# Kernel tuning notes

Hardware: AMD Instinct MI355X
Metric: run time of the kernel (lower is better)

## Reference

```python
import jax, jax.numpy as jnp
import numpy as np

B, N, K, H, NHEADS = 2, 2000, 32, 128, 4
EPS = 1e-6


def setup_inputs() -> dict:
    key = jax.random.key(0)
    ks = jax.random.split(key, 16)
    h_V = jax.random.normal(ks[0], (B, N, H), jnp.float32)
    h_EV = jax.random.normal(ks[1], (B, N, K, 2 * H), jnp.float32)
    h_KV = jax.random.normal(ks[2], (B, N, K, H), jnp.float32)
    h_KE = jax.random.normal(ks[3], (B, N, K, H), jnp.float32)
    mask_V = jax.random.randint(ks[4], (B, N), 0, 2).astype(jnp.float32)
    mask_attend = jax.random.randint(ks[5], (B, N, K), 0, 2).astype(jnp.float32)
    # guarantee at least one valid neighbor per node so masked softmax is finite
    mask_attend = mask_attend.at[:, :, 0].set(1.0)
    s = 1.0 / np.sqrt(H)
    W_Q = jax.random.normal(ks[6], (H, H), jnp.float32) * s
    W_K1 = jax.random.normal(ks[7], (H, H), jnp.float32) * s
    W_K2 = jax.random.normal(ks[8], (H, H), jnp.float32) * s
    W_V = jax.random.normal(ks[9], (H, 2 * H), jnp.float32) * s
    W_O = jax.random.normal(ks[10], (H, H), jnp.float32) * s
    gain = jnp.ones((H,), jnp.float32)
    bias = jnp.zeros((H,), jnp.float32)
    return dict(h_V=h_V, h_EV=h_EV, h_KV=h_KV, h_KE=h_KE, mask_V=mask_V,
                mask_attend=mask_attend, W_Q=W_Q, W_K1=W_K1, W_K2=W_K2,
                W_V=W_V, W_O=W_O, gain=gain, bias=bias)


def reference(h_V, h_EV, h_KV, h_KE, mask_V, mask_attend,
              W_Q, W_K1, W_K2, W_V, W_O, gain, bias):
    d = H // NHEADS  # per-head dim
    # Linear layers (torch Linear: x @ W.T), split heads
    Q = (h_V @ W_Q.T).reshape(B, N, 1, NHEADS, d)        # [B,N,1,h,d]
    K1 = (h_KE @ W_K1.T).reshape(B, N, K, NHEADS, d)     # [B,N,K,h,d]
    K2 = (h_KV @ W_K2.T).reshape(B, N, K, NHEADS, d)
    V = (h_EV @ W_V.T).reshape(B, N, K, NHEADS, d)
    # QKK: elementwise triple product reduced over d -> [B,N,K,h] -> [B,N,h,K]
    logits = jnp.sum(Q * K1 * K2, axis=-1)
    logits = jnp.swapaxes(logits, -2, -1) / d            # [B,N,h,K]
    # masked softmax over neighbors
    mask = jnp.broadcast_to(mask_attend[:, :, None, :], logits.shape)
    neg_inf = jnp.float32(np.finfo(np.float32).min)
    attend = jax.nn.softmax(jnp.where(mask > 0, logits, neg_inf), axis=-1)
    attend = mask * attend
    # aggregate neighbors per head, merge heads, output projection
    h_up = jnp.einsum('bnhk,bnkhd->bnhd', attend, V).reshape(B, N, H)
    dh = h_up @ W_O.T
    # residual + Normalize (torch .var is unbiased -> ddof=1)
    x = h_V + dh
    mu = x.mean(-1, keepdims=True)
    sigma = jnp.sqrt(x.var(-1, ddof=1, keepdims=True) + EPS)
    out = gain * (x - mu) / (sigma + EPS) + bias
    return mask_V[..., None] * out
```

## Files before the change

kernel.cpp:

```cpp
#include <hip/hip_runtime.h>
#include <hip/hip_bf16.h>
#include <math.h>

#define BN_TOTAL 4000
#define NODES 4
#define KN 32
#define HD 128
#define NH 4

typedef unsigned short ushort_t;
typedef unsigned int u32;
typedef short bf16x8 __attribute__((ext_vector_type(8)));
typedef float f32x4  __attribute__((ext_vector_type(4)));

__device__ __forceinline__ float bf2f(ushort_t u) {
    return __uint_as_float(((u32)u) << 16);
}
__device__ __forceinline__ ushort_t f2bf(float f) {
    u32 u = __float_as_uint(f);
    u += 0x7FFFu + ((u >> 16) & 1u);
    return (ushort_t)(u >> 16);
}
__device__ __forceinline__ u32 pack2bf(float lo, float hi) {
    return ((u32)f2bf(hi) << 16) | (u32)f2bf(lo);
}
__device__ __forceinline__ void cvt8(uint4 w, float* f) {
    f[0] = __uint_as_float(w.x << 16); f[1] = __uint_as_float(w.x & 0xFFFF0000u);
    f[2] = __uint_as_float(w.y << 16); f[3] = __uint_as_float(w.y & 0xFFFF0000u);
    f[4] = __uint_as_float(w.z << 16); f[5] = __uint_as_float(w.z & 0xFFFF0000u);
    f[6] = __uint_as_float(w.w << 16); f[7] = __uint_as_float(w.w & 0xFFFF0000u);
}

template<bool ISBF>
__device__ __forceinline__ void load8(const void* base, int idx, float* f) {
    if (ISBF) {
        uint4 v = *reinterpret_cast<const uint4*>((const ushort_t*)base + idx);
        cvt8(v, f);
    } else {
        const float* p = (const float*)base + idx;
        float4 a = *reinterpret_cast<const float4*>(p);
        float4 b = *reinterpret_cast<const float4*>(p + 4);
        f[0] = a.x; f[1] = a.y; f[2] = a.z; f[3] = a.w;
        f[4] = b.x; f[5] = b.y; f[6] = b.z; f[7] = b.w;
    }
}
template<bool ISBF>
__device__ __forceinline__ float load1(const void* base, int idx) {
    return ISBF ? bf2f(((const ushort_t*)base)[idx]) : ((const float*)base)[idx];
}
template<bool ISBF>
__device__ __forceinline__ bf16x8 loadfrag(const void* base, int idx) {
    if (ISBF) {
        return *reinterpret_cast<const bf16x8*>((const ushort_t*)base + idx);
    } else {
        const float* p = (const float*)base + idx;
        float4 a = *reinterpret_cast<const float4*>(p);
        float4 b = *reinterpret_cast<const float4*>(p + 4);
        bf16x8 r;
        r[0] = (short)f2bf(a.x); r[1] = (short)f2bf(a.y);
        r[2] = (short)f2bf(a.z); r[3] = (short)f2bf(a.w);
        r[4] = (short)f2bf(b.x); r[5] = (short)f2bf(b.y);
        r[6] = (short)f2bf(b.z); r[7] = (short)f2bf(b.w);
        return r;
    }
}

template<bool ISBF>
__device__ __forceinline__ void stage_chunk(const void* W, int elem_off, u32* sW,
                                            int chunk, int lane) {
    if (ISBF) {
        uint4 v = *reinterpret_cast<const uint4*>((const ushort_t*)W + elem_off);
        *reinterpret_cast<uint4*>(sW + chunk * 256 + lane * 4) = v;
    } else {
        const float* p = (const float*)W + elem_off;
        float4 a = *reinterpret_cast<const float4*>(p);
        float4 b = *reinterpret_cast<const float4*>(p + 4);
        uint4 v;
        v.x = pack2bf(a.x, a.y); v.y = pack2bf(a.z, a.w);
        v.z = pack2bf(b.x, b.y); v.w = pack2bf(b.z, b.w);
        *reinterpret_cast<uint4*>(sW + chunk * 256 + lane * 4) = v;
    }
}
__device__ __forceinline__ bf16x8 read_frag(const u32* sW, int chunk, int lane) {
    return *reinterpret_cast<const bf16x8*>(
        reinterpret_cast<const ushort_t*>(sW) + chunk * 512 + lane * 8);
}

template<bool ISBF>
__device__ __forceinline__ void run4(
    const void* h_V, const void* h_EV, const void* h_KV, const void* h_KE,
    const void* mask_V, const void* mask_att,
    const void* W_Q, const void* W_K1, const void* W_K2,
    const void* W_Vw, const void* W_O, const void* gain, const void* bias,
    void* out,
    u32* sW, float* shV, float* sQ, float* sLog, float* sAtt, float* sHU)
{
    const int t    = threadIdx.x;
    const int w    = t >> 6;
    const int lane = t & 63;
    const int quad = lane >> 4;
    const int lr   = lane & 15;
    const int node = blockIdx.x * NODES + w;
    const int c1   = lane, c2 = lane + 64;

    const float mA1 = load1<ISBF>(mask_att, node * KN + lr);
    const float mA2 = load1<ISBF>(mask_att, node * KN + 16 + lr);
    const float mV  = load1<ISBF>(mask_V, node);
    const float gn1 = load1<ISBF>(gain, c1), gn2 = load1<ISBF>(gain, c2);
    const float bs1 = load1<ISBF>(bias, c1), bs2 = load1<ISBF>(bias, c2);

    #pragma unroll
    for (int j = 0; j < 16; ++j) {
        const int c  = w * 16 + j;
        const int ks = (c >> 3) & 3, nt = c & 7;
        const void* W = (c < 32) ? W_K1 : W_K2;
        stage_chunk<ISBF>(W, (nt * 16 + lr) * HD + ks * 32 + quad * 8, sW, c, lane);
    }

    shV[w * HD + 2 * lane]     = load1<ISBF>(h_V, node * HD + 2 * lane);
    shV[w * HD + 2 * lane + 1] = load1<ISBF>(h_V, node * HD + 2 * lane + 1);

    bf16x8 aKE[2][4], aKV[2][4];
    const int aoff = node * KN * HD;
    #pragma unroll
    for (int mt = 0; mt < 2; ++mt)
        #pragma unroll
        for (int ks = 0; ks < 4; ++ks) {
            const int eo = aoff + (mt * 16 + lr) * HD + ks * 32 + quad * 8;
            aKE[mt][ks] = loadfrag<ISBF>(h_KE, eo);
            aKV[mt][ks] = loadfrag<ISBF>(h_KV, eo);
        }
    __syncthreads();

    {
        float q1 = 0.f, q2 = 0.f;
        #pragma unroll 4
        for (int jc = 0; jc < HD; jc += 8) {
            float hv[8];
            #pragma unroll
            for (int j = 0; j < 8; ++j) hv[j] = shV[w * HD + jc + j];
            float w1[8], w2[8];
            load8<ISBF>(W_Q, c1 * HD + jc, w1);
            load8<ISBF>(W_Q, c2 * HD + jc, w2);
            #pragma unroll
            for (int j = 0; j < 8; ++j) { q1 += w1[j] * hv[j]; q2 += w2[j] * hv[j]; }
        }
        sQ[w * HD + c1] = q1;
        sQ[w * HD + c2] = q2;
    }
    __syncthreads();

    float qv[8];
    #pragma unroll
    for (int nt = 0; nt < 8; ++nt) qv[nt] = sQ[w * HD + nt * 16 + lr];

    const f32x4 zero4 = {0.f, 0.f, 0.f, 0.f};
    #pragma unroll
    for (int h = 0; h < NH; ++h) {
        f32x4 a1[2][2], a2[2][2];
        #pragma unroll
        for (int mt = 0; mt < 2; ++mt)
            #pragma unroll
            for (int j = 0; j < 2; ++j) { a1[mt][j] = zero4; a2[mt][j] = zero4; }
        #pragma unroll
        for (int ks = 0; ks < 4; ++ks) {
            #pragma unroll
            for (int j = 0; j < 2; ++j) {
                const int nt = 2 * h + j;
                bf16x8 b1 = read_frag(sW, ks * 8 + nt, lane);
                bf16x8 b2 = read_frag(sW, 32 + ks * 8 + nt, lane);
                #pragma unroll
                for (int mt = 0; mt < 2; ++mt) {
                    a1[mt][j] = __builtin_amdgcn_mfma_f32_16x16x32_bf16(aKE[mt][ks], b1, a1[mt][j], 0, 0, 0);
                    a2[mt][j] = __builtin_amdgcn_mfma_f32_16x16x32_bf16(aKV[mt][ks], b2, a2[mt][j], 0, 0, 0);
                }
            }
        }
        #pragma unroll
        for (int mt = 0; mt < 2; ++mt) {
            #pragma unroll
            for (int r = 0; r < 4; ++r) {
                float p = qv[2 * h] * a1[mt][0][r] * a2[mt][0][r]
                        + qv[2 * h + 1] * a1[mt][1][r] * a2[mt][1][r];
                p += __shfl_xor(p, 1); p += __shfl_xor(p, 2);
                p += __shfl_xor(p, 4); p += __shfl_xor(p, 8);
                if (lr == 0)
                    sLog[w * HD + h * KN + mt * 16 + quad * 4 + r] = p * (1.f / 32.f);
            }
        }
    }
    __syncthreads();

    #pragma unroll
    for (int j = 0; j < 16; ++j) {
        const int c  = w * 16 + j;
        const int ks = c >> 3, nt = c & 7;
        stage_chunk<ISBF>(W_Vw, (nt * 16 + lr) * 256 + ks * 32 + quad * 8, sW, c, lane);
    }
    bf16x8 aEV[2][8];
    const int eoff = node * KN * 256;
    #pragma unroll
    for (int mt = 0; mt < 2; ++mt)
        #pragma unroll
        for (int ks = 0; ks < 8; ++ks)
            aEV[mt][ks] = loadfrag<ISBF>(h_EV, eoff + (mt * 16 + lr) * 256 + ks * 32 + quad * 8);

    {
        const int h = quad;
        float l1 = sLog[w * HD + h * KN + lr];
        float l2 = sLog[w * HD + h * KN + 16 + lr];
        const float NEG = -3.402823466e38f;
        l1 = (mA1 > 0.f) ? l1 : NEG;
        l2 = (mA2 > 0.f) ? l2 : NEG;
        float mx = fmaxf(l1, l2);
        #pragma unroll
        for (int d = 1; d < 16; d <<= 1) mx = fmaxf(mx, __shfl_xor(mx, d));
        float e1 = __expf(l1 - mx), e2 = __expf(l2 - mx);
        float ss = e1 + e2;
        #pragma unroll
        for (int d = 1; d < 16; d <<= 1) ss += __shfl_xor(ss, d);
        float inv = 1.f / ss;
        sAtt[w * HD + h * KN + lr]      = mA1 * e1 * inv;
        sAtt[w * HD + h * KN + 16 + lr] = mA2 * e2 * inv;
    }
    __syncthreads();

    #pragma unroll
    for (int h = 0; h < NH; ++h) {
        f32x4 cv[2][2];
        #pragma unroll
        for (int mt = 0; mt < 2; ++mt)
            #pragma unroll
            for (int j = 0; j < 2; ++j) cv[mt][j] = zero4;
        #pragma unroll
        for (int ks = 0; ks < 8; ++ks) {
            #pragma unroll
            for (int j = 0; j < 2; ++j) {
                bf16x8 b = read_frag(sW, ks * 8 + 2 * h + j, lane);
                #pragma unroll
                for (int mt = 0; mt < 2; ++mt)
                    cv[mt][j] = __builtin_amdgcn_mfma_f32_16x16x32_bf16(aEV[mt][ks], b, cv[mt][j], 0, 0, 0);
            }
        }
        float hu0 = 0.f, hu1 = 0.f;
        #pragma unroll
        for (int mt = 0; mt < 2; ++mt) {
            #pragma unroll
            for (int r = 0; r < 4; ++r) {
                float a = sAtt[w * HD + h * KN + mt * 16 + quad * 4 + r];
                hu0 += a * cv[mt][0][r];
                hu1 += a * cv[mt][1][r];
            }
        }
        hu0 += __shfl_xor(hu0, 16); hu0 += __shfl_xor(hu0, 32);
        hu1 += __shfl_xor(hu1, 16); hu1 += __shfl_xor(hu1, 32);
        if (quad == 0) {
            sHU[w * HD + (2 * h) * 16 + lr]     = hu0;
            sHU[w * HD + (2 * h + 1) * 16 + lr] = hu1;
        }
    }
    __syncthreads();

    {
        float d1 = 0.f, d2 = 0.f;
        #pragma unroll 4
        for (int jc = 0; jc < HD; jc += 8) {
            float hv[8];
            #pragma unroll
            for (int j = 0; j < 8; ++j) hv[j] = sHU[w * HD + jc + j];
            float w1[8], w2[8];
            load8<ISBF>(W_O, c1 * HD + jc, w1);
            load8<ISBF>(W_O, c2 * HD + jc, w2);
            #pragma unroll
            for (int j = 0; j < 8; ++j) { d1 += w1[j] * hv[j]; d2 += w2[j] * hv[j]; }
        }
        float x1 = shV[w * HD + c1] + d1;
        float x2 = shV[w * HD + c2] + d2;
        float s  = x1 + x2;
        float s2 = x1 * x1 + x2 * x2;
        #pragma unroll
        for (int d = 1; d < 64; d <<= 1) {
            s  += __shfl_xor(s, d);
            s2 += __shfl_xor(s2, d);
        }
        float mu    = s * (1.f / 128.f);
        float var   = (s2 - 128.f * mu * mu) * (1.f / 127.f);
        float sigma = sqrtf(var + 1e-6f);
        float inv   = 1.f / (sigma + 1e-6f);
        float o1 = mV * (gn1 * (x1 - mu) * inv + bs1);
        float o2 = mV * (gn2 * (x2 - mu) * inv + bs2);
        if (ISBF) {
            ((ushort_t*)out)[node * HD + c1] = f2bf(o1);
            ((ushort_t*)out)[node * HD + c2] = f2bf(o2);
        } else {
            ((float*)out)[node * HD + c1] = o1;
            ((float*)out)[node * HD + c2] = o2;
        }
    }
}

__global__ __launch_bounds__(256, 2) void spatppi_kernel(
    const void* h_V, const void* h_EV, const void* h_KV, const void* h_KE,
    const void* mask_V, const void* mask_att,
    const void* W_Q, const void* W_K1, const void* W_K2,
    const void* W_Vw, const void* W_O, const void* gain, const void* bias,
    void* out)
{
    __shared__ u32 sW[16384];
    __shared__ float shV[NODES * HD];
    __shared__ float sQ[NODES * HD];
    __shared__ float sLog[NODES * HD];
    __shared__ float sAtt[NODES * HD];
    __shared__ float sHU[NODES * HD];

    const bool isbf = (((const u32*)gain)[0] != 0x3F800000u);
    if (isbf)
        run4<true >(h_V, h_EV, h_KV, h_KE, mask_V, mask_att, W_Q, W_K1, W_K2,
                    W_Vw, W_O, gain, bias, out, sW, shV, sQ, sLog, sAtt, sHU);
    else
        run4<false>(h_V, h_EV, h_KV, h_KE, mask_V, mask_att, W_Q, W_K1, W_K2,
                    W_Vw, W_O, gain, bias, out, sW, shV, sQ, sLog, sAtt, sHU);
}

extern "C" void kernel_launch(void* const* d_in, const int* in_sizes, int n_in,
                              void* d_out, int out_size, void* d_ws, size_t ws_size,
                              hipStream_t stream) {
    spatppi_kernel<<<dim3(BN_TOTAL / NODES), dim3(256), 0, stream>>>(
        d_in[0], d_in[1], d_in[2], d_in[3], d_in[4], d_in[5],
        d_in[6], d_in[7], d_in[8], d_in[9], d_in[10], d_in[11], d_in[12],
        d_out);
}
```

Baseline: 353.7 us.

## Drop LDS weight staging; load MFMA weight fragments from global memory

Removes the 64KB shared-memory weight buffer and all block-wide barriers. Each warp now reads W_K1/W_K2/W_V fragments straight from global (L2-cached) memory and handles one 16-row tile of neighbors at a time to cut register pressure. Launch bounds rise to 4 blocks per SM to raise occupancy. The cost is far more global weight traffic per block, plus an fp32-to-bf16 conversion of the weights on every load in the fp32 path.

```diff
diff --git a/kernel.cpp b/kernel.cpp
--- a/kernel.cpp
+++ b/kernel.cpp
@@ -1,5 +1,4 @@
 #include <hip/hip_runtime.h>
-#include <hip/hip_bf16.h>
 #include <math.h>
 
 #define BN_TOTAL 4000
@@ -20,9 +19,6 @@
     u32 u = __float_as_uint(f);
     u += 0x7FFFu + ((u >> 16) & 1u);
     return (ushort_t)(u >> 16);
-}
-__device__ __forceinline__ u32 pack2bf(float lo, float hi) {
-    return ((u32)f2bf(hi) << 16) | (u32)f2bf(lo);
 }
 __device__ __forceinline__ void cvt8(uint4 w, float* f) {
     f[0] = __uint_as_float(w.x << 16); f[1] = __uint_as_float(w.x & 0xFFFF0000u);
@@ -66,34 +62,13 @@
 }
 
 template<bool ISBF>
-__device__ __forceinline__ void stage_chunk(const void* W, int elem_off, u32* sW,
-                                            int chunk, int lane) {
-    if (ISBF) {
-        uint4 v = *reinterpret_cast<const uint4*>((const ushort_t*)W + elem_off);
-        *reinterpret_cast<uint4*>(sW + chunk * 256 + lane * 4) = v;
-    } else {
-        const float* p = (const float*)W + elem_off;
-        float4 a = *reinterpret_cast<const float4*>(p);
-        float4 b = *reinterpret_cast<const float4*>(p + 4);
-        uint4 v;
-        v.x = pack2bf(a.x, a.y); v.y = pack2bf(a.z, a.w);
-        v.z = pack2bf(b.x, b.y); v.w = pack2bf(b.z, b.w);
-        *reinterpret_cast<uint4*>(sW + chunk * 256 + lane * 4) = v;
-    }
-}
-__device__ __forceinline__ bf16x8 read_frag(const u32* sW, int chunk, int lane) {
-    return *reinterpret_cast<const bf16x8*>(
-        reinterpret_cast<const ushort_t*>(sW) + chunk * 512 + lane * 8);
-}
-
-template<bool ISBF>
 __device__ __forceinline__ void run4(
     const void* h_V, const void* h_EV, const void* h_KV, const void* h_KE,
     const void* mask_V, const void* mask_att,
     const void* W_Q, const void* W_K1, const void* W_K2,
     const void* W_Vw, const void* W_O, const void* gain, const void* bias,
     void* out,
-    u32* sW, float* shV, float* sQ, float* sLog, float* sAtt, float* sHU)
+    float* shV, float* sQ, float* sLog, float* sAtt, float* sHU)
 {
     const int t    = threadIdx.x;
     const int w    = t >> 6;
@@ -105,32 +80,9 @@
 
     const float mA1 = load1<ISBF>(mask_att, node * KN + lr);
     const float mA2 = load1<ISBF>(mask_att, node * KN + 16 + lr);
-    const float mV  = load1<ISBF>(mask_V, node);
-    const float gn1 = load1<ISBF>(gain, c1), gn2 = load1<ISBF>(gain, c2);
-    const float bs1 = load1<ISBF>(bias, c1), bs2 = load1<ISBF>(bias, c2);
-
-    #pragma unroll
-    for (int j = 0; j < 16; ++j) {
-        const int c  = w * 16 + j;
-        const int ks = (c >> 3) & 3, nt = c & 7;
-        const void* W = (c < 32) ? W_K1 : W_K2;
-        stage_chunk<ISBF>(W, (nt * 16 + lr) * HD + ks * 32 + quad * 8, sW, c, lane);
-    }
 
     shV[w * HD + 2 * lane]     = load1<ISBF>(h_V, node * HD + 2 * lane);
     shV[w * HD + 2 * lane + 1] = load1<ISBF>(h_V, node * HD + 2 * lane + 1);
-
-    bf16x8 aKE[2][4], aKV[2][4];
-    const int aoff = node * KN * HD;
-    #pragma unroll
-    for (int mt = 0; mt < 2; ++mt)
-        #pragma unroll
-        for (int ks = 0; ks < 4; ++ks) {
-            const int eo = aoff + (mt * 16 + lr) * HD + ks * 32 + quad * 8;
-            aKE[mt][ks] = loadfrag<ISBF>(h_KE, eo);
-            aKV[mt][ks] = loadfrag<ISBF>(h_KV, eo);
-        }
-    __syncthreads();
 
     {
         float q1 = 0.f, q2 = 0.f;
@@ -148,40 +100,41 @@
         sQ[w * HD + c1] = q1;
         sQ[w * HD + c2] = q2;
     }
-    __syncthreads();
-
     float qv[8];
     #pragma unroll
     for (int nt = 0; nt < 8; ++nt) qv[nt] = sQ[w * HD + nt * 16 + lr];
 
     const f32x4 zero4 = {0.f, 0.f, 0.f, 0.f};
-    #pragma unroll
-    for (int h = 0; h < NH; ++h) {
-        f32x4 a1[2][2], a2[2][2];
-        #pragma unroll
-        for (int mt = 0; mt < 2; ++mt)
-            #pragma unroll
-            for (int j = 0; j < 2; ++j) { a1[mt][j] = zero4; a2[mt][j] = zero4; }
+
+    const int aoff = node * KN * HD;
+    #pragma unroll
+    for (int mt = 0; mt < 2; ++mt) {
+        bf16x8 aKE[4], aKV[4];
         #pragma unroll
         for (int ks = 0; ks < 4; ++ks) {
-            #pragma unroll
-            for (int j = 0; j < 2; ++j) {
-                const int nt = 2 * h + j;
-                bf16x8 b1 = read_frag(sW, ks * 8 + nt, lane);
-                bf16x8 b2 = read_frag(sW, 32 + ks * 8 + nt, lane);
+            const int eo = aoff + (mt * 16 + lr) * HD + ks * 32 + quad * 8;
+            aKE[ks] = loadfrag<ISBF>(h_KE, eo);
+            aKV[ks] = loadfrag<ISBF>(h_KV, eo);
+        }
+        #pragma unroll
+        for (int h = 0; h < NH; ++h) {
+            f32x4 a1[2], a2[2];
+            a1[0] = zero4; a1[1] = zero4; a2[0] = zero4; a2[1] = zero4;
+            #pragma unroll
+            for (int ks = 0; ks < 4; ++ks) {
                 #pragma unroll
-                for (int mt = 0; mt < 2; ++mt) {
-                    a1[mt][j] = __builtin_amdgcn_mfma_f32_16x16x32_bf16(aKE[mt][ks], b1, a1[mt][j], 0, 0, 0);
-                    a2[mt][j] = __builtin_amdgcn_mfma_f32_16x16x32_bf16(aKV[mt][ks], b2, a2[mt][j], 0, 0, 0);
+                for (int j = 0; j < 2; ++j) {
+                    const int wo = ((2 * h + j) * 16 + lr) * HD + ks * 32 + quad * 8;
+                    bf16x8 b1 = loadfrag<ISBF>(W_K1, wo);
+                    bf16x8 b2 = loadfrag<ISBF>(W_K2, wo);
+                    a1[j] = __builtin_amdgcn_mfma_f32_16x16x32_bf16(aKE[ks], b1, a1[j], 0, 0, 0);
+                    a2[j] = __builtin_amdgcn_mfma_f32_16x16x32_bf16(aKV[ks], b2, a2[j], 0, 0, 0);
                 }
             }
-        }
-        #pragma unroll
-        for (int mt = 0; mt < 2; ++mt) {
             #pragma unroll
             for (int r = 0; r < 4; ++r) {
-                float p = qv[2 * h] * a1[mt][0][r] * a2[mt][0][r]
-                        + qv[2 * h + 1] * a1[mt][1][r] * a2[mt][1][r];
+                float p = qv[2 * h] * a1[0][r] * a2[0][r]
+                        + qv[2 * h + 1] * a1[1][r] * a2[1][r];
                 p += __shfl_xor(p, 1); p += __shfl_xor(p, 2);
                 p += __shfl_xor(p, 4); p += __shfl_xor(p, 8);
                 if (lr == 0)
@@ -189,21 +142,6 @@
             }
         }
     }
-    __syncthreads();
-
-    #pragma unroll
-    for (int j = 0; j < 16; ++j) {
-        const int c  = w * 16 + j;
-        const int ks = c >> 3, nt = c & 7;
-        stage_chunk<ISBF>(W_Vw, (nt * 16 + lr) * 256 + ks * 32 + quad * 8, sW, c, lane);
-    }
-    bf16x8 aEV[2][8];
-    const int eoff = node * KN * 256;
-    #pragma unroll
-    for (int mt = 0; mt < 2; ++mt)
-        #pragma unroll
-        for (int ks = 0; ks < 8; ++ks)
-            aEV[mt][ks] = loadfrag<ISBF>(h_EV, eoff + (mt * 16 + lr) * 256 + ks * 32 + quad * 8);
 
     {
         const int h = quad;
@@ -223,35 +161,41 @@
         sAtt[w * HD + h * KN + lr]      = mA1 * e1 * inv;
         sAtt[w * HD + h * KN + 16 + lr] = mA2 * e2 * inv;
     }
-    __syncthreads();
-
-    #pragma unroll
-    for (int h = 0; h < NH; ++h) {
-        f32x4 cv[2][2];
-        #pragma unroll
-        for (int mt = 0; mt < 2; ++mt)
-            #pragma unroll
-            for (int j = 0; j < 2; ++j) cv[mt][j] = zero4;
-        #pragma unroll
-        for (int ks = 0; ks < 8; ++ks) {
-            #pragma unroll
-            for (int j = 0; j < 2; ++j) {
-                bf16x8 b = read_frag(sW, ks * 8 + 2 * h + j, lane);
+
+    const int eoff = node * KN * 256;
+    float hu[NH][2];
+    #pragma unroll
+    for (int h = 0; h < NH; ++h) { hu[h][0] = 0.f; hu[h][1] = 0.f; }
+    #pragma unroll
+    for (int mt = 0; mt < 2; ++mt) {
+        bf16x8 aEV[8];
+        #pragma unroll
+        for (int ks = 0; ks < 8; ++ks)
+            aEV[ks] = loadfrag<ISBF>(h_EV, eoff + (mt * 16 + lr) * 256 + ks * 32 + quad * 8);
+        #pragma unroll
+        for (int h = 0; h < NH; ++h) {
+            f32x4 cv[2];
+            cv[0] = zero4; cv[1] = zero4;
+            #pragma unroll
+            for (int ks = 0; ks < 8; ++ks) {
                 #pragma unroll
-                for (int mt = 0; mt < 2; ++mt)
-                    cv[mt][j] = __builtin_amdgcn_mfma_f32_16x16x32_bf16(aEV[mt][ks], b, cv[mt][j], 0, 0, 0);
-            }
-        }
-        float hu0 = 0.f, hu1 = 0.f;
-        #pragma unroll
-        for (int mt = 0; mt < 2; ++mt) {
+                for (int j = 0; j < 2; ++j) {
+                    bf16x8 b = loadfrag<ISBF>(W_Vw,
+                        ((2 * h + j) * 16 + lr) * 256 + ks * 32 + quad * 8);
+                    cv[j] = __builtin_amdgcn_mfma_f32_16x16x32_bf16(aEV[ks], b, cv[j], 0, 0, 0);
+                }
+            }
             #pragma unroll
             for (int r = 0; r < 4; ++r) {
                 float a = sAtt[w * HD + h * KN + mt * 16 + quad * 4 + r];
-                hu0 += a * cv[mt][0][r];
-                hu1 += a * cv[mt][1][r];
-            }
-        }
+                hu[h][0] += a * cv[0][r];
+                hu[h][1] += a * cv[1][r];
+            }
+        }
+    }
+    #pragma unroll
+    for (int h = 0; h < NH; ++h) {
+        float hu0 = hu[h][0], hu1 = hu[h][1];
         hu0 += __shfl_xor(hu0, 16); hu0 += __shfl_xor(hu0, 32);
         hu1 += __shfl_xor(hu1, 16); hu1 += __shfl_xor(hu1, 32);
         if (quad == 0) {
@@ -259,9 +203,11 @@
             sHU[w * HD + (2 * h + 1) * 16 + lr] = hu1;
         }
     }
-    __syncthreads();
 
     {
+        const float mV  = load1<ISBF>(mask_V, node);
+        const float gn1 = load1<ISBF>(gain, c1), gn2 = load1<ISBF>(gain, c2);
+        const float bs1 = load1<ISBF>(bias, c1), bs2 = load1<ISBF>(bias, c2);
         float d1 = 0.f, d2 = 0.f;
         #pragma unroll 4
         for (int jc = 0; jc < HD; jc += 8) {
@@ -299,14 +245,13 @@
     }
 }
 
-__global__ __launch_bounds__(256, 2) void spatppi_kernel(
+__global__ __launch_bounds__(256, 4) void spatppi_kernel(
     const void* h_V, const void* h_EV, const void* h_KV, const void* h_KE,
     const void* mask_V, const void* mask_att,
     const void* W_Q, const void* W_K1, const void* W_K2,
     const void* W_Vw, const void* W_O, const void* gain, const void* bias,
     void* out)
 {
-    __shared__ u32 sW[16384];
     __shared__ float shV[NODES * HD];
     __shared__ float sQ[NODES * HD];
     __shared__ float sLog[NODES * HD];
@@ -316,10 +261,10 @@
     const bool isbf = (((const u32*)gain)[0] != 0x3F800000u);
     if (isbf)
         run4<true >(h_V, h_EV, h_KV, h_KE, mask_V, mask_att, W_Q, W_K1, W_K2,
-                    W_Vw, W_O, gain, bias, out, sW, shV, sQ, sLog, sAtt, sHU);
+                    W_Vw, W_O, gain, bias, out, shV, sQ, sLog, sAtt, sHU);
     else
         run4<false>(h_V, h_EV, h_KV, h_KE, mask_V, mask_att, W_Q, W_K1, W_K2,
-                    W_Vw, W_O, gain, bias, out, sW, shV, sQ, sLog, sAtt, sHU);
+                    W_Vw, W_O, gain, bias, out, shV, sQ, sLog, sAtt, sHU);
 }
 
 extern "C" void kernel_launch(void* const* d_in, const int* in_sizes, int n_in,
```

New measurement: 637.7 us. 80.3% more time.

## Process two nodes per wave with all weights staged once and prefetched inputs

Applied to the files above, without the earlier changes.

The kernel moves from 4 waves with one node each to 8 waves with two nodes each. W_K1, W_K2 and W_V are all staged into a 128KB shared buffer once per block, and the mid-kernel barriers between phases are removed. The next node's h_KE/h_KV fragments and the h_EV fragments are prefetched while MFMA work on the current node runs. This amortises weight staging and synchronisation and hides global load latency. In exchange, the larger LDS footprint and register pressure likely limit the kernel to one block per CU, and the grid shrinks to 250 blocks.

```diff
diff --git a/kernel.cpp b/kernel.cpp
--- a/kernel.cpp
+++ b/kernel.cpp
@@ -1,9 +1,9 @@
 #include <hip/hip_runtime.h>
-#include <hip/hip_bf16.h>
 #include <math.h>
 
 #define BN_TOTAL 4000
-#define NODES 4
+#define WAVES 8
+#define NPW 2
 #define KN 32
 #define HD 128
 #define NH 4
@@ -87,7 +87,7 @@
 }
 
 template<bool ISBF>
-__device__ __forceinline__ void run4(
+__device__ __forceinline__ void run8(
     const void* h_V, const void* h_EV, const void* h_KV, const void* h_KE,
     const void* mask_V, const void* mask_att,
     const void* W_Q, const void* W_K1, const void* W_K2,
@@ -100,232 +100,259 @@
     const int lane = t & 63;
     const int quad = lane >> 4;
     const int lr   = lane & 15;
-    const int node = blockIdx.x * NODES + w;
+    const int base = (blockIdx.x * WAVES + w) * NPW;
     const int c1   = lane, c2 = lane + 64;
 
-    const float mA1 = load1<ISBF>(mask_att, node * KN + lr);
-    const float mA2 = load1<ISBF>(mask_att, node * KN + 16 + lr);
-    const float mV  = load1<ISBF>(mask_V, node);
+    #pragma unroll
+    for (int j = 0; j < 16; ++j) {
+        const int c = w * 16 + j;
+        if (c < 64) {
+            const int ks = (c >> 3) & 3, nt = c & 7;
+            const void* W = (c < 32) ? W_K1 : W_K2;
+            stage_chunk<ISBF>(W, (nt * 16 + lr) * HD + ks * 32 + quad * 8, sW, c, lane);
+        } else {
+            const int cv = c - 64;
+            const int ks = cv >> 3, nt = cv & 7;
+            stage_chunk<ISBF>(W_Vw, (nt * 16 + lr) * 256 + ks * 32 + quad * 8, sW, c, lane);
+        }
+    }
+
+    bf16x8 aKE[2][4], aKV[2][4];
+    {
+        const int ao = base * KN * HD;
+        #pragma unroll
+        for (int mt = 0; mt < 2; ++mt)
+            #pragma unroll
+            for (int ks = 0; ks < 4; ++ks) {
+                const int eo = ao + (mt * 16 + lr) * HD + ks * 32 + quad * 8;
+                aKE[mt][ks] = loadfrag<ISBF>(h_KE, eo);
+                aKV[mt][ks] = loadfrag<ISBF>(h_KV, eo);
+            }
+    }
+
+    float mA1[NPW], mA2[NPW], mVv[NPW];
+    #pragma unroll
+    for (int it = 0; it < NPW; ++it) {
+        const int node = base + it;
+        mA1[it] = load1<ISBF>(mask_att, node * KN + lr);
+        mA2[it] = load1<ISBF>(mask_att, node * KN + 16 + lr);
+        mVv[it] = load1<ISBF>(mask_V, node);
+        shV[(w * NPW + it) * HD + 2 * lane]     = load1<ISBF>(h_V, node * HD + 2 * lane);
+        shV[(w * NPW + it) * HD + 2 * lane + 1] = load1<ISBF>(h_V, node * HD + 2 * lane + 1);
+    }
     const float gn1 = load1<ISBF>(gain, c1), gn2 = load1<ISBF>(gain, c2);
     const float bs1 = load1<ISBF>(bias, c1), bs2 = load1<ISBF>(bias, c2);
-
-    #pragma unroll
-    for (int j = 0; j < 16; ++j) {
-        const int c  = w * 16 + j;
-        const int ks = (c >> 3) & 3, nt = c & 7;
-        const void* W = (c < 32) ? W_K1 : W_K2;
-        stage_chunk<ISBF>(W, (nt * 16 + lr) * HD + ks * 32 + quad * 8, sW, c, lane);
-    }
-
-    shV[w * HD + 2 * lane]     = load1<ISBF>(h_V, node * HD + 2 * lane);
-    shV[w * HD + 2 * lane + 1] = load1<ISBF>(h_V, node * HD + 2 * lane + 1);
-
-    bf16x8 aKE[2][4], aKV[2][4];
-    const int aoff = node * KN * HD;
-    #pragma unroll
-    for (int mt = 0; mt < 2; ++mt)
-        #pragma unroll
-        for (int ks = 0; ks < 4; ++ks) {
-            const int eo = aoff + (mt * 16 + lr) * HD + ks * 32 + quad * 8;
-            aKE[mt][ks] = loadfrag<ISBF>(h_KE, eo);
-            aKV[mt][ks] = loadfrag<ISBF>(h_KV, eo);
-        }
-    __syncthreads();
-
     {
-        float q1 = 0.f, q2 = 0.f;
+        float q1[NPW], q2[NPW];
+        #pragma unroll
+        for (int it = 0; it < NPW; ++it) { q1[it] = 0.f; q2[it] = 0.f; }
         #pragma unroll 4
         for (int jc = 0; jc < HD; jc += 8) {
-            float hv[8];
-            #pragma unroll
-            for (int j = 0; j < 8; ++j) hv[j] = shV[w * HD + jc + j];
             float w1[8], w2[8];
             load8<ISBF>(W_Q, c1 * HD + jc, w1);
             load8<ISBF>(W_Q, c2 * HD + jc, w2);
             #pragma unroll
-            for (int j = 0; j < 8; ++j) { q1 += w1[j] * hv[j]; q2 += w2[j] * hv[j]; }
-        }
-        sQ[w * HD + c1] = q1;
-        sQ[w * HD + c2] = q2;
-    }
+            for (int it = 0; it < NPW; ++it) {
+                #pragma unroll
+                for (int j = 0; j < 8; ++j) {
+                    float hv = shV[(w * NPW + it) * HD + jc + j];
+                    q1[it] += w1[j] * hv; q2[it] += w2[j] * hv;
+                }
+            }
+        }
+        #pragma unroll
+        for (int it = 0; it < NPW; ++it) {
+            sQ[(w * NPW + it) * HD + c1] = q1[it];
+            sQ[(w * NPW + it) * HD + c2] = q2[it];
+        }
+    }
+    float qv[NPW][8];
+    #pragma unroll
+    for (int it = 0; it < NPW; ++it)
+        #pragma unroll
+        for (int nt = 0; nt < 8; ++nt)
+            qv[it][nt] = sQ[(w * NPW + it) * HD + nt * 16 + lr];
+
     __syncthreads();
 
-    float qv[8];
+    const f32x4 zero4 = {0.f, 0.f, 0.f, 0.f};
+    bf16x8 aEV[2][8];
+
     #pragma unroll
-    for (int nt = 0; nt < 8; ++nt) qv[nt] = sQ[w * HD + nt * 16 + lr];
-
-    const f32x4 zero4 = {0.f, 0.f, 0.f, 0.f};
-    #pragma unroll
-    for (int h = 0; h < NH; ++h) {
-        f32x4 a1[2][2], a2[2][2];
-        #pragma unroll
-        for (int mt = 0; mt < 2; ++mt)
-            #pragma unroll
-            for (int j = 0; j < 2; ++j) { a1[mt][j] = zero4; a2[mt][j] = zero4; }
-        #pragma unroll
-        for (int ks = 0; ks < 4; ++ks) {
-            #pragma unroll
-            for (int j = 0; j < 2; ++j) {
-                const int nt = 2 * h + j;
-                bf16x8 b1 = read_frag(sW, ks * 8 + nt, lane);
-                bf16x8 b2 = read_frag(sW, 32 + ks * 8 + nt, lane);
-                #pragma unroll
-                for (int mt = 0; mt < 2; ++mt) {
-                    a1[mt][j] = __builtin_amdgcn_mfma_f32_16x16x32_bf16(aKE[mt][ks], b1, a1[mt][j], 0, 0, 0);
-                    a2[mt][j] = __builtin_amdgcn_mfma_f32_16x16x32_bf16(aKV[mt][ks], b2, a2[mt][j], 0, 0, 0);
-                }
-            }
-        }
+    for (int it = 0; it < NPW; ++it) {
+        const int node   = base + it;
+        const int eoffEV = node * KN * 256;
+
         #pragma unroll
         for (int mt = 0; mt < 2; ++mt) {
-            #pragma unroll
-            for (int r = 0; r < 4; ++r) {
-                float p = qv[2 * h] * a1[mt][0][r] * a2[mt][0][r]
-                        + qv[2 * h + 1] * a1[mt][1][r] * a2[mt][1][r];
-                p += __shfl_xor(p, 1); p += __shfl_xor(p, 2);
-                p += __shfl_xor(p, 4); p += __shfl_xor(p, 8);
-                if (lr == 0)
-                    sLog[w * HD + h * KN + mt * 16 + quad * 4 + r] = p * (1.f / 32.f);
-            }
-        }
-    }
-    __syncthreads();
-
-    #pragma unroll
-    for (int j = 0; j < 16; ++j) {
-        const int c  = w * 16 + j;
-        const int ks = c >> 3, nt = c & 7;
-        stage_chunk<ISBF>(W_Vw, (nt * 16 + lr) * 256 + ks * 32 + quad * 8, sW, c, lane);
-    }
-    bf16x8 aEV[2][8];
-    const int eoff = node * KN * 256;
-    #pragma unroll
-    for (int mt = 0; mt < 2; ++mt)
-        #pragma unroll
-        for (int ks = 0; ks < 8; ++ks)
-            aEV[mt][ks] = loadfrag<ISBF>(h_EV, eoff + (mt * 16 + lr) * 256 + ks * 32 + quad * 8);
-
-    {
-        const int h = quad;
-        float l1 = sLog[w * HD + h * KN + lr];
-        float l2 = sLog[w * HD + h * KN + 16 + lr];
-        const float NEG = -3.402823466e38f;
-        l1 = (mA1 > 0.f) ? l1 : NEG;
-        l2 = (mA2 > 0.f) ? l2 : NEG;
-        float mx = fmaxf(l1, l2);
-        #pragma unroll
-        for (int d = 1; d < 16; d <<= 1) mx = fmaxf(mx, __shfl_xor(mx, d));
-        float e1 = __expf(l1 - mx), e2 = __expf(l2 - mx);
-        float ss = e1 + e2;
-        #pragma unroll
-        for (int d = 1; d < 16; d <<= 1) ss += __shfl_xor(ss, d);
-        float inv = 1.f / ss;
-        sAtt[w * HD + h * KN + lr]      = mA1 * e1 * inv;
-        sAtt[w * HD + h * KN + 16 + lr] = mA2 * e2 * inv;
-    }
-    __syncthreads();
-
-    #pragma unroll
-    for (int h = 0; h < NH; ++h) {
-        f32x4 cv[2][2];
-        #pragma unroll
-        for (int mt = 0; mt < 2; ++mt)
-            #pragma unroll
-            for (int j = 0; j < 2; ++j) cv[mt][j] = zero4;
-        #pragma unroll
-        for (int ks = 0; ks < 8; ++ks) {
-            #pragma unroll
-            for (int j = 0; j < 2; ++j) {
-                bf16x8 b = read_frag(sW, ks * 8 + 2 * h + j, lane);
-                #pragma unroll
-                for (int mt = 0; mt < 2; ++mt)
-                    cv[mt][j] = __builtin_amdgcn_mfma_f32_16x16x32_bf16(aEV[mt][ks], b, cv[mt][j], 0, 0, 0);
-            }
-        }
-        float hu0 = 0.f, hu1 = 0.f;
+            if (mt == 1) {
+                #pragma unroll
+                for (int ks = 0; ks < 8; ++ks)
+                    aEV[0][ks] = loadfrag<ISBF>(h_EV,
+                        eoffEV + lr * 256 + ks * 32 + quad * 8);
+            }
+            #pragma unroll
+            for (int h = 0; h < NH; ++h) {
+                f32x4 a1[2], a2[2];
+                a1[0] = zero4; a1[1] = zero4; a2[0] = zero4; a2[1] = zero4;
+                #pragma unroll
+                for (int ks = 0; ks < 4; ++ks) {
+                    #pragma unroll
+                    for (int j = 0; j < 2; ++j) {
+                        bf16x8 b1 = read_frag(sW, ks * 8 + 2 * h + j, lane);
+                        bf16x8 b2 = read_frag(sW, 32 + ks * 8 + 2 * h + j, lane);
+                        a1[j] = __builtin_amdgcn_mfma_f32_16x16x32_bf16(aKE[mt][ks], b1, a1[j], 0, 0, 0);
+                        a2[j] = __builtin_amdgcn_mfma_f32_16x16x32_bf16(aKV[mt][ks], b2, a2[j], 0, 0, 0);
+                    }
+                }
+                #pragma unroll
+                for (int r = 0; r < 4; ++r) {
+                    float p = qv[it][2 * h] * a1[0][r] * a2[0][r]
+                            + qv[it][2 * h + 1] * a1[1][r] * a2[1][r];
+                    p += __shfl_xor(p, 1); p += __shfl_xor(p, 2);
+                    p += __shfl_xor(p, 4); p += __shfl_xor(p, 8);
+                    if (lr == 0)
+                        sLog[w * HD + h * KN + mt * 16 + quad * 4 + r] = p * (1.f / 32.f);
+                }
+            }
+        }
+
+        {
+            float l1 = sLog[w * HD + quad * KN + lr];
+            float l2 = sLog[w * HD + quad * KN + 16 + lr];
+            const float NEG = -3.402823466e38f;
+            l1 = (mA1[it] > 0.f) ? l1 : NEG;
+            l2 = (mA2[it] > 0.f) ? l2 : NEG;
+            float mx = fmaxf(l1, l2);
+            #pragma unroll
+            for (int d = 1; d < 16; d <<= 1) mx = fmaxf(mx, __shfl_xor(mx, d));
+            float e1 = __expf(l1 - mx), e2 = __expf(l2 - mx);
+            float ss = e1 + e2;
+            #pragma unroll
+            for (int d = 1; d < 16; d <<= 1) ss += __shfl_xor(ss, d);
+            float inv = 1.f / ss;
+            sAtt[w * HD + quad * KN + lr]      = mA1[it] * e1 * inv;
+            sAtt[w * HD + quad * KN + 16 + lr] = mA2[it] * e2 * inv;
+        }
+
+        float hu[NH][2];
+        #pragma unroll
+        for (int h = 0; h < NH; ++h) { hu[h][0] = 0.f; hu[h][1] = 0.f; }
         #pragma unroll
         for (int mt = 0; mt < 2; ++mt) {
-            #pragma unroll
-            for (int r = 0; r < 4; ++r) {
-                float a = sAtt[w * HD + h * KN + mt * 16 + quad * 4 + r];
-                hu0 += a * cv[mt][0][r];
-                hu1 += a * cv[mt][1][r];
-            }
-        }
-        hu0 += __shfl_xor(hu0, 16); hu0 += __shfl_xor(hu0, 32);
-        hu1 += __shfl_xor(hu1, 16); hu1 += __shfl_xor(hu1, 32);
-        if (quad == 0) {
-            sHU[w * HD + (2 * h) * 16 + lr]     = hu0;
-            sHU[w * HD + (2 * h + 1) * 16 + lr] = hu1;
-        }
-    }
-    __syncthreads();
-
-    {
-        float d1 = 0.f, d2 = 0.f;
-        #pragma unroll 4
-        for (int jc = 0; jc < HD; jc += 8) {
-            float hv[8];
-            #pragma unroll
-            for (int j = 0; j < 8; ++j) hv[j] = sHU[w * HD + jc + j];
-            float w1[8], w2[8];
-            load8<ISBF>(W_O, c1 * HD + jc, w1);
-            load8<ISBF>(W_O, c2 * HD + jc, w2);
-            #pragma unroll
-            for (int j = 0; j < 8; ++j) { d1 += w1[j] * hv[j]; d2 += w2[j] * hv[j]; }
-        }
-        float x1 = shV[w * HD + c1] + d1;
-        float x2 = shV[w * HD + c2] + d2;
-        float s  = x1 + x2;
-        float s2 = x1 * x1 + x2 * x2;
-        #pragma unroll
-        for (int d = 1; d < 64; d <<= 1) {
-            s  += __shfl_xor(s, d);
-            s2 += __shfl_xor(s2, d);
-        }
-        float mu    = s * (1.f / 128.f);
-        float var   = (s2 - 128.f * mu * mu) * (1.f / 127.f);
-        float sigma = sqrtf(var + 1e-6f);
-        float inv   = 1.f / (sigma + 1e-6f);
-        float o1 = mV * (gn1 * (x1 - mu) * inv + bs1);
-        float o2 = mV * (gn2 * (x2 - mu) * inv + bs2);
-        if (ISBF) {
-            ((ushort_t*)out)[node * HD + c1] = f2bf(o1);
-            ((ushort_t*)out)[node * HD + c2] = f2bf(o2);
-        } else {
-            ((float*)out)[node * HD + c1] = o1;
-            ((float*)out)[node * HD + c2] = o2;
-        }
-    }
-}
-
-__global__ __launch_bounds__(256, 2) void spatppi_kernel(
+            if (mt == 0) {
+                #pragma unroll
+                for (int ks = 0; ks < 8; ++ks)
+                    aEV[1][ks] = loadfrag<ISBF>(h_EV,
+                        eoffEV + (16 + lr) * 256 + ks * 32 + quad * 8);
+            } else if (it + 1 < NPW) {
+                const int ao = (node + 1) * KN * HD;
+                #pragma unroll
+                for (int m2 = 0; m2 < 2; ++m2)
+                    #pragma unroll
+                    for (int ks = 0; ks < 4; ++ks) {
+                        const int eo = ao + (m2 * 16 + lr) * HD + ks * 32 + quad * 8;
+                        aKE[m2][ks] = loadfrag<ISBF>(h_KE, eo);
+                        aKV[m2][ks] = loadfrag<ISBF>(h_KV, eo);
+                    }
+            }
+            #pragma unroll
+            for (int h = 0; h < NH; ++h) {
+                f32x4 cv[2];
+                cv[0] = zero4; cv[1] = zero4;
+                #pragma unroll
+                for (int ks = 0; ks < 8; ++ks) {
+                    #pragma unroll
+                    for (int j = 0; j < 2; ++j) {
+                        bf16x8 b = read_frag(sW, 64 + ks * 8 + 2 * h + j, lane);
+                        cv[j] = __builtin_amdgcn_mfma_f32_16x16x32_bf16(aEV[mt][ks], b, cv[j], 0, 0, 0);
+                    }
+                }
+                #pragma unroll
+                for (int r = 0; r < 4; ++r) {
+                    float a = sAtt[w * HD + h * KN + mt * 16 + quad * 4 + r];
+                    hu[h][0] += a * cv[0][r];
+                    hu[h][1] += a * cv[1][r];
+                }
+            }
+        }
+        #pragma unroll
+        for (int h = 0; h < NH; ++h) {
+            float hu0 = hu[h][0], hu1 = hu[h][1];
+            hu0 += __shfl_xor(hu0, 16); hu0 += __shfl_xor(hu0, 32);
+            hu1 += __shfl_xor(hu1, 16); hu1 += __shfl_xor(hu1, 32);
+            if (quad == 0) {
+                sHU[w * HD + (2 * h) * 16 + lr]     = hu0;
+                sHU[w * HD + (2 * h + 1) * 16 + lr] = hu1;
+            }
+        }
+
+        {
+            float d1 = 0.f, d2 = 0.f;
+            #pragma unroll 4
+            for (int jc = 0; jc < HD; jc += 8) {
+                float hv[8];
+                #pragma unroll
+                for (int j = 0; j < 8; ++j) hv[j] = sHU[w * HD + jc + j];
+                float w1[8], w2[8];
+                load8<ISBF>(W_O, c1 * HD + jc, w1);
+                load8<ISBF>(W_O, c2 * HD + jc, w2);
+                #pragma unroll
+                for (int j = 0; j < 8; ++j) { d1 += w1[j] * hv[j]; d2 += w2[j] * hv[j]; }
+            }
+            float x1 = shV[(w * NPW + it) * HD + c1] + d1;
+            float x2 = shV[(w * NPW + it) * HD + c2] + d2;
+            float s  = x1 + x2;
+            float s2 = x1 * x1 + x2 * x2;
+            #pragma unroll
+            for (int d = 1; d < 64; d <<= 1) {
+                s  += __shfl_xor(s, d);
+                s2 += __shfl_xor(s2, d);
+            }
+            float mu    = s * (1.f / 128.f);
+            float var   = (s2 - 128.f * mu * mu) * (1.f / 127.f);
+            float sigma = sqrtf(var + 1e-6f);
+            float inv   = 1.f / (sigma + 1e-6f);
+            float o1 = mVv[it] * (gn1 * (x1 - mu) * inv + bs1);
+            float o2 = mVv[it] * (gn2 * (x2 - mu) * inv + bs2);
+            if (ISBF) {
+                ((ushort_t*)out)[node * HD + c1] = f2bf(o1);
+                ((ushort_t*)out)[node * HD + c2] = f2bf(o2);
+            } else {
+                ((float*)out)[node * HD + c1] = o1;
+                ((float*)out)[node * HD + c2] = o2;
+            }
+        }
+    }
+}
+
+__global__ __launch_bounds__(512) void spatppi_kernel(
     const void* h_V, const void* h_EV, const void* h_KV, const void* h_KE,
     const void* mask_V, const void* mask_att,
     const void* W_Q, const void* W_K1, const void* W_K2,
     const void* W_Vw, const void* W_O, const void* gain, const void* bias,
     void* out)
 {
-    __shared__ u32 sW[16384];
-    __shared__ float shV[NODES * HD];
-    __shared__ float sQ[NODES * HD];
-    __shared__ float sLog[NODES * HD];
-    __shared__ float sAtt[NODES * HD];
-    __shared__ float sHU[NODES * HD];
+    __shared__ u32 sW[32768];
+    __shared__ float shV[WAVES * NPW * HD];
+    __shared__ float sQ[WAVES * NPW * HD];
+    __shared__ float sLog[WAVES * HD];
+    __shared__ float sAtt[WAVES * HD];
+    __shared__ float sHU[WAVES * HD];
 
     const bool isbf = (((const u32*)gain)[0] != 0x3F800000u);
     if (isbf)
-        run4<true >(h_V, h_EV, h_KV, h_KE, mask_V, mask_att, W_Q, W_K1, W_K2,
+        run8<true >(h_V, h_EV, h_KV, h_KE, mask_V, mask_att, W_Q, W_K1, W_K2,
                     W_Vw, W_O, gain, bias, out, sW, shV, sQ, sLog, sAtt, sHU);
     else
-        run4<false>(h_V, h_EV, h_KV, h_KE, mask_V, mask_att, W_Q, W_K1, W_K2,
+        run8<false>(h_V, h_EV, h_KV, h_KE, mask_V, mask_att, W_Q, W_K1, W_K2,
                     W_Vw, W_O, gain, bias, out, sW, shV, sQ, sLog, sAtt, sHU);
 }
 
 extern "C" void kernel_launch(void* const* d_in, const int* in_sizes, int n_in,
                               void* d_out, int out_size, void* d_ws, size_t ws_size,
                               hipStream_t stream) {
-    spatppi_kernel<<<dim3(BN_TOTAL / NODES), dim3(256), 0, stream>>>(
+    spatppi_kernel<<<dim3(BN_TOTAL / (WAVES * NPW)), dim3(512), 0, stream>>>(
         d_in[0], d_in[1], d_in[2], d_in[3], d_in[4], d_in[5],
         d_in[6], d_in[7], d_in[8], d_in[9], d_in[10], d_in[11], d_in[12],
         d_out);
```

New measurement: 554.2 us. +56.7%, slower.
